# Performance work log

Hardware: AMD Instinct MI355X
Metric: run time of the kernel (lower is better)

The kernel has to match this reference:

```python
import jax, jax.numpy as jnp
import numpy as np

D_MODEL = 128
D_STATE = 256
D_CONV = 4
EXPAND = 2
D_INNER = EXPAND * D_MODEL  # 256 == D_STATE (required by the module's einsum/add)
B = 4
L = 100  # fixed: self.C has first dim 100


def silu(x):
    return x * jax.nn.sigmoid(x)


def setup_inputs() -> dict:
    key = jax.random.key(0)
    ks = jax.random.split(key, 10)
    s = 0.02
    dt_std = D_INNER ** (-0.5)
    inp = {
        "hidden_states": jax.random.normal(ks[0], (B, L, D_MODEL), jnp.float32),
        "state": jax.random.normal(ks[1], (B, L, D_INNER, D_STATE), jnp.float32),
        # torch nn.Linear layout: (out_features, in_features)
        "in_proj_w": jax.random.normal(ks[2], (2 * D_INNER, D_MODEL), jnp.float32) * s,
        "in_proj_b": jnp.zeros((2 * D_INNER,), jnp.float32),
        # depthwise conv1d weight: (d_inner, 1, d_conv)
        "conv_w": jax.random.normal(ks[3], (D_INNER, 1, D_CONV), jnp.float32) * s,
        "conv_b": jnp.zeros((D_INNER,), jnp.float32),
        "x_proj_w": jax.random.normal(ks[4], (2 * D_STATE, D_INNER), jnp.float32) * s,
        "dt_proj_w": jax.random.uniform(ks[5], (D_INNER, D_INNER), jnp.float32, -dt_std, dt_std),
        "dt_proj_b": jnp.zeros((D_INNER,), jnp.float32),
        # A_log = log(arange(1, d_state+1)) broadcast to (d_inner, d_state)
        "A_log": jnp.log(jnp.broadcast_to(jnp.arange(1, D_STATE + 1, dtype=jnp.float32), (D_INNER, D_STATE))),
        "D1": jnp.ones((D_INNER,), jnp.float32),
        # torch inits self.C to ones; add tiny noise to avoid degenerate baseline
        "C_param": jnp.ones((L, D_STATE, D_STATE), jnp.float32) + jax.random.normal(ks[6], (L, D_STATE, D_STATE), jnp.float32) * 0.01,
        "out_proj_w": jax.random.normal(ks[7], (D_MODEL, D_INNER), jnp.float32) * s,
        "out_proj_b": jnp.zeros((D_MODEL,), jnp.float32),
    }
    return inp


def reference(hidden_states, state, in_proj_w, in_proj_b, conv_w, conv_b,
              x_proj_w, dt_proj_w, dt_proj_b, A_log, D1, C_param,
              out_proj_w, out_proj_b):
    b, l, _ = hidden_states.shape
    xz = hidden_states @ in_proj_w.T + in_proj_b          # (b, l, 2*d_inner)
    x, z = jnp.split(xz, 2, axis=-1)                      # each (b, l, d_inner)

    # causal depthwise conv: pad (d_conv-1) left == conv with pad both sides then [:, :, :l]
    xc = jnp.transpose(x, (0, 2, 1))                      # (b, d_inner, l)
    xc = jax.lax.conv_general_dilated(
        xc, conv_w, window_strides=(1,), padding=[(conv_w.shape[-1] - 1, 0)],
        dimension_numbers=("NCH", "OIH", "NCH"), feature_group_count=xc.shape[1])
    xc = xc + conv_b[None, :, None]
    x = silu(jnp.transpose(xc, (0, 2, 1)))                # (b, l, d_inner)

    bc = x @ x_proj_w.T                                   # (b, l, 2*d_state)
    Bm, _Cm_unused = jnp.split(bc, 2, axis=-1)            # torch shadows chunked C with self.C

    dt = jax.nn.softplus(x @ dt_proj_w.T + dt_proj_b)     # (b, l, d_inner)
    A = -jnp.exp(A_log)                                   # (d_inner, d_state)
    dA = jnp.exp(dt[..., None] * A)                       # (b, l, d_inner, d_state)
    dB = dt[..., None] * Bm[..., None, :]                 # (b, l, d_inner, d_state)
    actual_state = state * dA + dB                        # elementwise 'blnd,blnd->blnd'

    y = jnp.einsum("bldn,ldn->bln", actual_state, C_param) + D1 * x  # (b, l, d_inner)
    y = y * silu(z)
    out = y @ out_proj_w.T + out_proj_b                   # (b, l, d_model)
    return out, actual_state
```

## Files before the change

### kernel.cpp

```cpp
#include <hip/hip_runtime.h>

#define LEN 100
#define NR 400

__device__ __forceinline__ float siluf_(float x) { return x / (1.0f + __expf(-x)); }
__device__ __forceinline__ float softplusf_(float x) {
    return (x > 20.f) ? x : log1pf(expf(x));
}

typedef float f4v __attribute__((ext_vector_type(4)));
__device__ __forceinline__ float4 nt_load4(const float* p) {
    f4v t = __builtin_nontemporal_load((const f4v*)p);
    return make_float4(t.x, t.y, t.z, t.w);
}
__device__ __forceinline__ void nt_store4(float* p, float4 v) {
    f4v t; t.x = v.x; t.y = v.y; t.z = v.z; t.w = v.w;
    __builtin_nontemporal_store(t, (f4v*)p);
}

__global__ void __launch_bounds__(256) k_front(
    const float* __restrict__ hidden, const float* __restrict__ ipw, const float* __restrict__ ipb,
    const float* __restrict__ cw, const float* __restrict__ cb,
    const float* __restrict__ xpw, const float* __restrict__ dtw, const float* __restrict__ dtb,
    float* __restrict__ xact, float* __restrict__ Bm, float* __restrict__ dt,
    float* __restrict__ zs)
{
    int l = blockIdx.x;
    int j = threadIdx.x;
    int lb = l < 3 ? l : 3;
    __shared__ __align__(16) float hid[4][4][128];
    __shared__ __align__(16) float xs[4][256];

    for (int e = j; e < 2048; e += 256) {
        int b = e >> 9;
        int k = (e >> 7) & 3;
        int c = e & 127;
        int r = b * LEN + l;
        hid[b][k][c] = (k <= lb) ? hidden[(size_t)(r - k) * 128 + c] : 0.f;
    }
    __syncthreads();

    float b0 = ipb[j];
    float bz = ipb[256 + j];
    float xp[4][4];
    float zz[4];
#pragma unroll
    for (int b = 0; b < 4; ++b) {
        xp[b][0] = b0; xp[b][1] = b0; xp[b][2] = b0; xp[b][3] = b0;
        zz[b] = bz;
    }
    const float* wx = ipw + (size_t)j * 128;
    const float* wz = ipw + (size_t)(256 + j) * 128;
#pragma unroll 4
    for (int c = 0; c < 128; c += 4) {
        float4 w = *(const float4*)(wx + c);
        float4 v = *(const float4*)(wz + c);
#pragma unroll
        for (int b = 0; b < 4; ++b) {
            float4 h0 = *(const float4*)(&hid[b][0][c]);
            float4 h1 = *(const float4*)(&hid[b][1][c]);
            float4 h2 = *(const float4*)(&hid[b][2][c]);
            float4 h3 = *(const float4*)(&hid[b][3][c]);
            xp[b][0] += w.x * h0.x + w.y * h0.y + w.z * h0.z + w.w * h0.w;
            xp[b][1] += w.x * h1.x + w.y * h1.y + w.z * h1.z + w.w * h1.w;
            xp[b][2] += w.x * h2.x + w.y * h2.y + w.z * h2.z + w.w * h2.w;
            xp[b][3] += w.x * h3.x + w.y * h3.y + w.z * h3.z + w.w * h3.w;
            zz[b]    += v.x * h0.x + v.y * h0.y + v.z * h0.z + v.w * h0.w;
        }
    }

    float4 w4 = *(const float4*)(cw + j * 4);
    float cbj = cb[j];
#pragma unroll
    for (int b = 0; b < 4; ++b) {
        float conv = cbj + w4.w * xp[b][0];
        if (lb >= 1) conv += w4.z * xp[b][1];
        if (lb >= 2) conv += w4.y * xp[b][2];
        if (lb >= 3) conv += w4.x * xp[b][3];
        float xa = siluf_(conv);
        xs[b][j] = xa;
        int r = b * LEN + l;
        xact[r * 256 + j] = xa;
        zs[r * 256 + j] = siluf_(zz[b]);
    }
    __syncthreads();

    float accB[4], accD[4];
    float dtbj = dtb[j];
#pragma unroll
    for (int b = 0; b < 4; ++b) { accB[b] = 0.f; accD[b] = dtbj; }
    const float* bw = xpw + (size_t)j * 256;
    const float* dw = dtw + (size_t)j * 256;
#pragma unroll 8
    for (int c = 0; c < 256; c += 4) {
        float4 bwv = *(const float4*)(bw + c);
        float4 dwv = *(const float4*)(dw + c);
#pragma unroll
        for (int b = 0; b < 4; ++b) {
            float4 xv = *(const float4*)(&xs[b][c]);
            accB[b] += bwv.x * xv.x + bwv.y * xv.y + bwv.z * xv.z + bwv.w * xv.w;
            accD[b] += dwv.x * xv.x + dwv.y * xv.y + dwv.z * xv.z + dwv.w * xv.w;
        }
    }
#pragma unroll
    for (int b = 0; b < 4; ++b) {
        int r = b * LEN + l;
        Bm[r * 256 + j] = accB[b];
        dt[r * 256 + j] = softplusf_(accD[b]);
    }
}

__global__ void __launch_bounds__(256, 4) k_scan(
    const float* __restrict__ state, const float* __restrict__ alog,
    const float* __restrict__ Cp, const float* __restrict__ dtg,
    const float* __restrict__ Bm, float* __restrict__ ostate, float* __restrict__ ypart)
{
    int bid = blockIdx.x;
    int l = bid >> 4, sl = bid & 15;
    int tid = threadIdx.x;
    int wid = tid >> 6, lane = tid & 63, n0 = lane * 4;
    int d0 = sl * 16 + wid * 4;

    const float* cp = Cp + ((size_t)(l * 256 + d0)) * 256 + n0;
    const float* ap = alog + (size_t)d0 * 256 + n0;

    float4 Bv[4], dtq[4], acc[4];
    size_t soff[4];
#pragma unroll
    for (int b = 0; b < 4; ++b) {
        int r = b * LEN + l;
        Bv[b] = *(const float4*)(Bm + r * 256 + n0);
        dtq[b] = *(const float4*)(dtg + r * 256 + d0);
        soff[b] = ((size_t)(r * 256 + d0)) * 256 + n0;
        acc[b] = make_float4(0.f, 0.f, 0.f, 0.f);
    }

#pragma unroll
    for (int i = 0; i < 4; ++i) {
        float4 av = *(const float4*)(ap + (size_t)i * 256);
        float4 cv = nt_load4(cp + (size_t)i * 256);
        float4 na;
        na.x = -__expf(av.x); na.y = -__expf(av.y);
        na.z = -__expf(av.z); na.w = -__expf(av.w);
#pragma unroll
        for (int b = 0; b < 4; ++b) {
            float dtv = (i == 0) ? dtq[b].x : (i == 1) ? dtq[b].y
                      : (i == 2) ? dtq[b].z : dtq[b].w;
            float4 s = nt_load4(state + soff[b] + (size_t)i * 256);
            float4 as;
            as.x = s.x * __expf(dtv * na.x) + dtv * Bv[b].x;
            as.y = s.y * __expf(dtv * na.y) + dtv * Bv[b].y;
            as.z = s.z * __expf(dtv * na.z) + dtv * Bv[b].z;
            as.w = s.w * __expf(dtv * na.w) + dtv * Bv[b].w;
            nt_store4(ostate + soff[b] + (size_t)i * 256, as);
            acc[b].x += as.x * cv.x;
            acc[b].y += as.y * cv.y;
            acc[b].z += as.z * cv.z;
            acc[b].w += as.w * cv.w;
        }
    }

    __shared__ __align__(16) float accs[4][4][256];
#pragma unroll
    for (int b = 0; b < 4; ++b)
        *(float4*)(&accs[wid][b][n0]) = acc[b];
    __syncthreads();
    {
        float4 t0 = *(const float4*)(&accs[0][wid][n0]);
        float4 t1 = *(const float4*)(&accs[1][wid][n0]);
        float4 t2 = *(const float4*)(&accs[2][wid][n0]);
        float4 t3 = *(const float4*)(&accs[3][wid][n0]);
        float4 o;
        o.x = (t0.x + t1.x) + (t2.x + t3.x);
        o.y = (t0.y + t1.y) + (t2.y + t3.y);
        o.z = (t0.z + t1.z) + (t2.z + t3.z);
        o.w = (t0.w + t1.w) + (t2.w + t3.w);
        *(float4*)(ypart + ((size_t)(sl * NR + wid * LEN + l)) * 256 + n0) = o;
    }
}

__global__ void __launch_bounds__(256) k_back(
    const float* __restrict__ ypart, const float* __restrict__ xact,
    const float* __restrict__ zs, const float* __restrict__ D1,
    const float* __restrict__ ow, const float* __restrict__ ob,
    float* __restrict__ out)
{
    int l = blockIdx.x;
    int t = threadIdx.x;
    __shared__ __align__(16) float ys[4][256];
    __shared__ float ph[4][256];
    const int S = NR * 256;
    float d1 = D1[t];
#pragma unroll
    for (int b = 0; b < 4; ++b) {
        int idx = (b * LEN + l) * 256 + t;
        float v = 0.f;
#pragma unroll
        for (int q = 0; q < 16; q++) v += ypart[q * S + idx];
        v += d1 * xact[idx];
        v *= zs[idx];
        ys[b][t] = v;
    }
    __syncthreads();
    {
        int j = t & 127;
        int h = t >> 7;
        const float* wp = ow + (size_t)j * 256 + h * 128;
        float bias = (h == 0) ? ob[j] : 0.f;
        float acc[4];
#pragma unroll
        for (int b = 0; b < 4; ++b) acc[b] = bias;
#pragma unroll 8
        for (int c = 0; c < 128; c += 4) {
            float4 w = *(const float4*)(wp + c);
#pragma unroll
            for (int b = 0; b < 4; ++b) {
                float4 x = *(const float4*)(&ys[b][h * 128 + c]);
                acc[b] += w.x * x.x + w.y * x.y + w.z * x.z + w.w * x.w;
            }
        }
#pragma unroll
        for (int b = 0; b < 4; ++b) ph[b][t] = acc[b];
    }
    __syncthreads();
    if (t < 128) {
#pragma unroll
        for (int b = 0; b < 4; ++b)
            out[((size_t)(b * LEN + l)) * 128 + t] = ph[b][t] + ph[b][t + 128];
    }
}

extern "C" void kernel_launch(void* const* d_in, const int* in_sizes, int n_in,
                              void* d_out, int out_size, void* d_ws, size_t ws_size,
                              hipStream_t stream) {
    const float* hidden = (const float*)d_in[0];
    const float* state  = (const float*)d_in[1];
    const float* ipw    = (const float*)d_in[2];
    const float* ipb    = (const float*)d_in[3];
    const float* cw     = (const float*)d_in[4];
    const float* cb     = (const float*)d_in[5];
    const float* xpw    = (const float*)d_in[6];
    const float* dtw    = (const float*)d_in[7];
    const float* dtb    = (const float*)d_in[8];
    const float* alog   = (const float*)d_in[9];
    const float* D1     = (const float*)d_in[10];
    const float* Cp     = (const float*)d_in[11];
    const float* opw    = (const float*)d_in[12];
    const float* opb    = (const float*)d_in[13];

    float* out    = (float*)d_out;
    float* ostate = out + 51200;

    float* ws    = (float*)d_ws;
    float* xact  = ws;
    float* Bm    = ws + 102400;
    float* dt    = ws + 204800;
    float* zs    = ws + 307200;
    float* ypart = ws + 409600;

    k_front<<<100, 256, 0, stream>>>(hidden, ipw, ipb, cw, cb, xpw, dtw, dtb,
                                     xact, Bm, dt, zs);
    k_scan <<<1600, 256, 0, stream>>>(state, alog, Cp, dt, Bm, ostate, ypart);
    k_back <<<100, 256, 0, stream>>>(ypart, xact, zs, D1, opw, opb, out);
}
```

Baseline: 281.1 us.

## Transpose projection weights on device for coalesced loads in front/back kernels

Adds a transpose kernel that writes transposed copies of the in_proj, x_proj, dt_proj and out_proj weights into workspace on every call. The front and back kernels then read weights column-wise, so adjacent threads load adjacent addresses instead of striding by a full weight row per thread. Shared-memory activations are repacked as float4 across batch, so each activation read serves all four batches. It adds an extra launch and about 1 MB of weight traffic per call, and relies on the workspace being large enough at the new offsets.

```diff
diff --git a/kernel.cpp b/kernel.cpp
--- a/kernel.cpp
+++ b/kernel.cpp
@@ -18,25 +18,54 @@
     __builtin_nontemporal_store(t, (f4v*)p);
 }
 
+__global__ void __launch_bounds__(256) k_tr(
+    const float* __restrict__ ipw, const float* __restrict__ xpw,
+    const float* __restrict__ dtw, const float* __restrict__ ow,
+    float* __restrict__ ipwT, float* __restrict__ xpwT,
+    float* __restrict__ dtwT, float* __restrict__ owT)
+{
+    __shared__ float tile[32][33];
+    int bid = blockIdx.x;
+    const float* src; float* dst; int C; int tr, tc;
+    if (bid < 64)       { src = ipw; dst = ipwT; C = 128; int t = bid;       tr = t >> 2; tc = t & 3; }
+    else if (bid < 128) { src = xpw; dst = xpwT; C = 256; int t = bid - 64;  tr = t >> 3; tc = t & 7; }
+    else if (bid < 192) { src = dtw; dst = dtwT; C = 256; int t = bid - 128; tr = t >> 3; tc = t & 7; }
+    else                { src = ow;  dst = owT;  C = 256; int t = bid - 192; tr = t >> 3; tc = t & 7; }
+    int R = (bid < 64) ? 512 : (bid < 192 ? 256 : 128);
+    int r0 = tr * 32, c0 = tc * 32;
+    int tx = threadIdx.x & 31, ty = threadIdx.x >> 5;
+#pragma unroll
+    for (int k = 0; k < 32; k += 8)
+        tile[ty + k][tx] = src[(size_t)(r0 + ty + k) * C + c0 + tx];
+    __syncthreads();
+#pragma unroll
+    for (int k = 0; k < 32; k += 8)
+        dst[(size_t)(c0 + ty + k) * R + r0 + tx] = tile[tx][ty + k];
+}
+
 __global__ void __launch_bounds__(256) k_front(
-    const float* __restrict__ hidden, const float* __restrict__ ipw, const float* __restrict__ ipb,
+    const float* __restrict__ hidden, const float* __restrict__ ipwT, const float* __restrict__ ipb,
     const float* __restrict__ cw, const float* __restrict__ cb,
-    const float* __restrict__ xpw, const float* __restrict__ dtw, const float* __restrict__ dtb,
+    const float* __restrict__ xpwT, const float* __restrict__ dtwT, const float* __restrict__ dtb,
     float* __restrict__ xact, float* __restrict__ Bm, float* __restrict__ dt,
     float* __restrict__ zs)
 {
     int l = blockIdx.x;
     int j = threadIdx.x;
     int lb = l < 3 ? l : 3;
-    __shared__ __align__(16) float hid[4][4][128];
-    __shared__ __align__(16) float xs[4][256];
-
-    for (int e = j; e < 2048; e += 256) {
-        int b = e >> 9;
-        int k = (e >> 7) & 3;
+    __shared__ __align__(16) float4 hid4[4][128];
+    __shared__ __align__(16) float4 xs4[256];
+
+    for (int e = j; e < 512; e += 256) {
+        int b = e >> 7;
         int c = e & 127;
-        int r = b * LEN + l;
-        hid[b][k][c] = (k <= lb) ? hidden[(size_t)(r - k) * 128 + c] : 0.f;
+        size_t base = ((size_t)(b * LEN + l)) * 128 + c;
+        float4 h;
+        h.x = hidden[base];
+        h.y = (lb >= 1) ? hidden[base - 128] : 0.f;
+        h.z = (lb >= 2) ? hidden[base - 256] : 0.f;
+        h.w = (lb >= 3) ? hidden[base - 384] : 0.f;
+        hid4[b][c] = h;
     }
     __syncthreads();
 
@@ -49,28 +78,24 @@
         xp[b][0] = b0; xp[b][1] = b0; xp[b][2] = b0; xp[b][3] = b0;
         zz[b] = bz;
     }
-    const float* wx = ipw + (size_t)j * 128;
-    const float* wz = ipw + (size_t)(256 + j) * 128;
 #pragma unroll 4
-    for (int c = 0; c < 128; c += 4) {
-        float4 w = *(const float4*)(wx + c);
-        float4 v = *(const float4*)(wz + c);
+    for (int c = 0; c < 128; ++c) {
+        float w = ipwT[(size_t)c * 512 + j];
+        float v = ipwT[(size_t)c * 512 + 256 + j];
 #pragma unroll
         for (int b = 0; b < 4; ++b) {
-            float4 h0 = *(const float4*)(&hid[b][0][c]);
-            float4 h1 = *(const float4*)(&hid[b][1][c]);
-            float4 h2 = *(const float4*)(&hid[b][2][c]);
-            float4 h3 = *(const float4*)(&hid[b][3][c]);
-            xp[b][0] += w.x * h0.x + w.y * h0.y + w.z * h0.z + w.w * h0.w;
-            xp[b][1] += w.x * h1.x + w.y * h1.y + w.z * h1.z + w.w * h1.w;
-            xp[b][2] += w.x * h2.x + w.y * h2.y + w.z * h2.z + w.w * h2.w;
-            xp[b][3] += w.x * h3.x + w.y * h3.y + w.z * h3.z + w.w * h3.w;
-            zz[b]    += v.x * h0.x + v.y * h0.y + v.z * h0.z + v.w * h0.w;
+            float4 h = hid4[b][c];
+            xp[b][0] += w * h.x;
+            xp[b][1] += w * h.y;
+            xp[b][2] += w * h.z;
+            xp[b][3] += w * h.w;
+            zz[b]    += v * h.x;
         }
     }
 
     float4 w4 = *(const float4*)(cw + j * 4);
     float cbj = cb[j];
+    float4 xa4;
 #pragma unroll
     for (int b = 0; b < 4; ++b) {
         float conv = cbj + w4.w * xp[b][0];
@@ -78,29 +103,25 @@
         if (lb >= 2) conv += w4.y * xp[b][2];
         if (lb >= 3) conv += w4.x * xp[b][3];
         float xa = siluf_(conv);
-        xs[b][j] = xa;
         int r = b * LEN + l;
         xact[r * 256 + j] = xa;
         zs[r * 256 + j] = siluf_(zz[b]);
-    }
+        ((float*)&xa4)[b] = xa;
+    }
+    xs4[j] = xa4;
     __syncthreads();
 
     float accB[4], accD[4];
     float dtbj = dtb[j];
 #pragma unroll
     for (int b = 0; b < 4; ++b) { accB[b] = 0.f; accD[b] = dtbj; }
-    const float* bw = xpw + (size_t)j * 256;
-    const float* dw = dtw + (size_t)j * 256;
-#pragma unroll 8
-    for (int c = 0; c < 256; c += 4) {
-        float4 bwv = *(const float4*)(bw + c);
-        float4 dwv = *(const float4*)(dw + c);
-#pragma unroll
-        for (int b = 0; b < 4; ++b) {
-            float4 xv = *(const float4*)(&xs[b][c]);
-            accB[b] += bwv.x * xv.x + bwv.y * xv.y + bwv.z * xv.z + bwv.w * xv.w;
-            accD[b] += dwv.x * xv.x + dwv.y * xv.y + dwv.z * xv.z + dwv.w * xv.w;
-        }
+#pragma unroll 4
+    for (int c = 0; c < 256; ++c) {
+        float wb = xpwT[(size_t)c * 256 + j];
+        float wd = dtwT[(size_t)c * 256 + j];
+        float4 x = xs4[c];
+        accB[0] += wb * x.x; accB[1] += wb * x.y; accB[2] += wb * x.z; accB[3] += wb * x.w;
+        accD[0] += wd * x.x; accD[1] += wd * x.y; accD[2] += wd * x.z; accD[3] += wd * x.w;
     }
 #pragma unroll
     for (int b = 0; b < 4; ++b) {
@@ -182,15 +203,16 @@
 __global__ void __launch_bounds__(256) k_back(
     const float* __restrict__ ypart, const float* __restrict__ xact,
     const float* __restrict__ zs, const float* __restrict__ D1,
-    const float* __restrict__ ow, const float* __restrict__ ob,
+    const float* __restrict__ owT, const float* __restrict__ ob,
     float* __restrict__ out)
 {
     int l = blockIdx.x;
     int t = threadIdx.x;
-    __shared__ __align__(16) float ys[4][256];
+    __shared__ __align__(16) float4 ys4[256];
     __shared__ float ph[4][256];
     const int S = NR * 256;
     float d1 = D1[t];
+    float4 yv;
 #pragma unroll
     for (int b = 0; b < 4; ++b) {
         int idx = (b * LEN + l) * 256 + t;
@@ -199,25 +221,23 @@
         for (int q = 0; q < 16; q++) v += ypart[q * S + idx];
         v += d1 * xact[idx];
         v *= zs[idx];
-        ys[b][t] = v;
-    }
+        ((float*)&yv)[b] = v;
+    }
+    ys4[t] = yv;
     __syncthreads();
     {
-        int j = t & 127;
+        int jj = t & 127;
         int h = t >> 7;
-        const float* wp = ow + (size_t)j * 256 + h * 128;
-        float bias = (h == 0) ? ob[j] : 0.f;
+        float bias = (h == 0) ? ob[jj] : 0.f;
         float acc[4];
 #pragma unroll
         for (int b = 0; b < 4; ++b) acc[b] = bias;
-#pragma unroll 8
-        for (int c = 0; c < 128; c += 4) {
-            float4 w = *(const float4*)(wp + c);
-#pragma unroll
-            for (int b = 0; b < 4; ++b) {
-                float4 x = *(const float4*)(&ys[b][h * 128 + c]);
-                acc[b] += w.x * x.x + w.y * x.y + w.z * x.z + w.w * x.w;
-            }
+        int c0 = h * 128;
+#pragma unroll 4
+        for (int c = c0; c < c0 + 128; ++c) {
+            float w = owT[(size_t)c * 128 + jj];
+            float4 x = ys4[c];
+            acc[0] += w * x.x; acc[1] += w * x.y; acc[2] += w * x.z; acc[3] += w * x.w;
         }
 #pragma unroll
         for (int b = 0; b < 4; ++b) ph[b][t] = acc[b];
@@ -257,9 +277,14 @@
     float* dt    = ws + 204800;
     float* zs    = ws + 307200;
     float* ypart = ws + 409600;
-
-    k_front<<<100, 256, 0, stream>>>(hidden, ipw, ipb, cw, cb, xpw, dtw, dtb,
-                                     xact, Bm, dt, zs);
+    float* ipwT  = ws + 2048000;
+    float* xpwT  = ws + 2113536;
+    float* dtwT  = ws + 2179072;
+    float* owT   = ws + 2244608;
+
+    k_tr   <<<224,  256, 0, stream>>>(ipw, xpw, dtw, opw, ipwT, xpwT, dtwT, owT);
+    k_front<<<100,  256, 0, stream>>>(hidden, ipwT, ipb, cw, cb, xpwT, dtwT, dtb,
+                                      xact, Bm, dt, zs);
     k_scan <<<1600, 256, 0, stream>>>(state, alog, Cp, dt, Bm, ostate, ypart);
-    k_back <<<100, 256, 0, stream>>>(ypart, xact, zs, D1, opw, opb, out);
-}
+    k_back <<<100,  256, 0, stream>>>(ypart, xact, zs, D1, owT, opb, out);
+}
```

New measurement: 273.7 us. -2.6%, faster.
